# Optimization experiments

Measured on AMD Instinct MI355X. Metric: run time of the kernel, lower is better.

The kernel has to match this reference:

```python
import jax, jax.numpy as jnp
import numpy as np
import math

OUT_H, OUT_W = 608 // 4, 1088 // 4   # 152, 272
HW = OUT_H * OUT_W                   # 41344
MAX_OBJS = 256
N_ANN = 64
NID = 537
EMB_DIM = 256
EMB_SCALE = math.sqrt(2.0) * math.log(NID - 1.0)
B = 8


def gaussian_radius(height, width, min_overlap=0.7):
    # standard CenterNet radius; height/width are jnp.ceil'd box sizes
    b1 = height + width
    c1 = width * height * (1.0 - min_overlap) / (1.0 + min_overlap)
    r1 = (b1 + jnp.sqrt(jnp.maximum(b1 * b1 - 4.0 * c1, 0.0))) / 2.0
    b2 = 2.0 * (height + width)
    c2 = (1.0 - min_overlap) * width * height
    r2 = (b2 + jnp.sqrt(jnp.maximum(b2 * b2 - 16.0 * c2, 0.0))) / 2.0
    b3 = -2.0 * min_overlap * (height + width)
    c3 = (min_overlap - 1.0) * width * height
    r3 = (b3 + jnp.sqrt(jnp.maximum(b3 * b3 - 16.0 * min_overlap * c3, 0.0))) / 2.0
    return jnp.minimum(jnp.minimum(r1, r2), r3)


def build_targets(ann1, ann2):
    # ann cols: [cx, cy, w, h, cls, pid, vis, extra]; boxes normalized to [0,1]
    cx_raw = ann1[:, 0] * OUT_W
    cy_raw = ann1[:, 1] * OUT_H
    w = ann1[:, 2] * OUT_W
    h = ann1[:, 3] * OUT_H
    # amodal box from UNclipped center (torch deepcopies before clipping)
    x1 = cx_raw - 0.5 * w; y1 = cy_raw - 0.5 * h
    x2 = x1 + w;           y2 = y1 + h
    cx = jnp.clip(cx_raw, 0.0, OUT_W - 1.0)
    cy = jnp.clip(cy_raw, 0.0, OUT_H - 1.0)
    ctx = cx.astype(jnp.int32)
    cty = cy.astype(jnp.int32)
    radius = jnp.maximum(jnp.floor(gaussian_radius(jnp.ceil(h), jnp.ceil(w))), 0.0)

    # batched gaussian splat, max-reduced over objects (draw_umich_gaussian)
    sigma = (2.0 * radius + 1.0) / 6.0
    dx = jnp.arange(OUT_W, dtype=jnp.float32)[None, :] - ctx[:, None].astype(jnp.float32)  # [N,W]
    dy = jnp.arange(OUT_H, dtype=jnp.float32)[None, :] - cty[:, None].astype(jnp.float32)  # [N,H]
    g = jnp.exp(-(dy[:, :, None] ** 2 + dx[:, None, :] ** 2) / (2.0 * sigma[:, None, None] ** 2))  # [N,H,W]
    win = (jnp.abs(dy)[:, :, None] <= radius[:, None, None]) & (jnp.abs(dx)[:, None, :] <= radius[:, None, None])
    hm = jnp.max(jnp.where(win, g, 0.0), axis=0)  # [H,W]

    # first match of each object's pid in the next frame (torch breaks at first hit)
    pid1 = ann1[:, 5]
    match = pid1[:, None] == ann2[None, :, 5]
    has = match.any(axis=1)
    t1 = ann2[jnp.argmax(match, axis=1)]
    cx2 = t1[:, 0] * OUT_W; cy2 = t1[:, 1] * OUT_H
    w2 = t1[:, 2] * OUT_W;  h2 = t1[:, 3] * OUT_H
    x1t = cx2 - 0.5 * w2; y1t = cy2 - 0.5 * h2
    x2t = x1t + w2;       y2t = y1t + h2

    valid = has & (h > 0) & (w > 0) & (h2 > 0) & (w2 > 0)
    vm = valid.astype(jnp.float32)
    cxf = ctx.astype(jnp.float32); cyf = cty.astype(jnp.float32)
    wh = jnp.stack([cxf - x1, x2 - cxf, cyf - y1, y2 - cyf,
                    cxf - x1t, x2t - cxf, cyf - y1t, y2t - cyf], axis=-1) * vm[:, None]
    ind = jnp.where(valid, cty * OUT_W + ctx, 0)
    v = ann1[:, 6] * vm
    ids = jnp.where(valid, pid1.astype(jnp.int32), 0)

    pad = MAX_OBJS - N_ANN
    return (hm,
            jnp.pad(ind, (0, pad)),
            jnp.pad(vm, (0, pad)),
            jnp.pad(wh, ((0, pad), (0, 0))),
            jnp.pad(v, (0, pad)),
            jnp.pad(ids, (0, pad)))


def focal_loss(pred, gt):
    # CenterNet focal loss; pred already sigmoid+clamped
    pos = (gt == 1.0).astype(pred.dtype)
    pos_loss = (jnp.log(pred) * (1.0 - pred) ** 2 * pos).sum()
    neg_loss = (jnp.log(1.0 - pred) * pred ** 2 * (1.0 - gt) ** 4 * (1.0 - pos)).sum()
    num_pos = pos.sum()
    return jnp.where(num_pos > 0, -(pos_loss + neg_loss) / jnp.maximum(num_pos, 1.0), -neg_loss)


def reg_loss(feat, mask, ind, target):
    # feat [C,HW]; gather per-object channels, masked smooth-L1 sum / num_valid
    pred = feat[:, ind].T                       # [max_objs, C]
    m = mask[:, None]
    d = jnp.abs(pred * m - target * m)
    sl1 = jnp.where(d < 1.0, 0.5 * d * d, d - 0.5)
    return sl1.sum() / (mask.sum() + 1e-4)


def id_loss(identi, ind, mask, v, ids, W_id, b_id):
    feat = identi[:, ind].T                     # [max_objs, 256]
    feat = EMB_SCALE * feat / jnp.maximum(jnp.linalg.norm(feat, axis=-1, keepdims=True), 1e-12)
    logits = feat @ W_id.T + b_id               # [max_objs, 537]
    logp = jax.nn.log_softmax(logits, axis=-1)
    nll = -v * jnp.take_along_axis(logp, ids[:, None], axis=1)[:, 0]
    return (nll * mask).sum() / jnp.maximum(mask.sum(), 1.0)


def reference(classifications, regressions, viss, identis, annotations1, annotations2, W_id, b_id, s_det, s_id):
    cls = jnp.clip(jax.nn.sigmoid(classifications), 1e-4, 1.0 - 1e-4)   # [B,1,HW]
    vis = jnp.clip(jax.nn.sigmoid(viss), 1e-4, 1.0 - 1e-4)              # [B,1,HW]
    hm, ind, mask, wh, v, ids = jax.vmap(build_targets)(annotations1, annotations2)
    cls_l = jax.vmap(lambda p, g: focal_loss(p.reshape(OUT_H, OUT_W), g))(cls, hm)
    reg_l = jax.vmap(reg_loss)(regressions, mask, ind, wh)
    vis_l = jax.vmap(lambda f, m, i, t: reg_loss(f, m, i, t[:, None]))(vis, mask, ind, v)
    id_l = jax.vmap(lambda f, i, m, vv, ii: id_loss(f, i, m, vv, ii, W_id, b_id))(identis, ind, mask, v, ids)
    return (cls_l.mean(keepdims=True), reg_l.mean(keepdims=True), vis_l.mean(keepdims=True),
            id_l.mean(keepdims=True), s_det, s_id)


def setup_inputs() -> dict:
    key = jax.random.key(0)
    ks = jax.random.split(key, 8)
    classifications = jax.random.normal(ks[0], (B, 1, HW), dtype=jnp.float32)
    regressions = jax.random.normal(ks[1], (B, 8, HW), dtype=jnp.float32)
    viss = jax.random.normal(ks[2], (B, 1, HW), dtype=jnp.float32)
    identis = jax.random.normal(ks[3], (B, EMB_DIM, HW), dtype=jnp.float32)

    def make_frame_pair(k):
        k1, k2, k3, k4, k5, k6, k7 = jax.random.split(k, 7)
        cx = jax.random.uniform(k1, (N_ANN,), minval=0.05, maxval=0.95)
        cy = jax.random.uniform(k2, (N_ANN,), minval=0.05, maxval=0.95)
        w = jax.random.uniform(k3, (N_ANN,), minval=0.02, maxval=0.25)
        h = jax.random.uniform(k4, (N_ANN,), minval=0.05, maxval=0.4)
        pid = jax.random.permutation(k5, NID)[:N_ANN].astype(jnp.float32)  # unique track ids
        vis = jax.random.uniform(k6, (N_ANN,))
        extra = jax.random.uniform(k7, (N_ANN,))
        cls = jnp.zeros((N_ANN,), dtype=jnp.float32)
        a1 = jnp.stack([cx, cy, w, h, cls, pid, vis, extra], axis=-1)
        kp, kj = jax.random.split(jax.random.fold_in(k, 99))
        a2 = a1[jax.random.permutation(kp, N_ANN)]
        a2 = a2.at[:, 0:2].add(0.01 * jax.random.normal(kj, (N_ANN, 2)))
        a2 = a2.at[:, 0:2].set(jnp.clip(a2[:, 0:2], 0.05, 0.95))
        return a1, a2

    pairs = [make_frame_pair(jax.random.fold_in(ks[4], b)) for b in range(B)]
    annotations1 = jnp.stack([p[0] for p in pairs])
    annotations2 = jnp.stack([p[1] for p in pairs])
    W_id = 0.02 * jax.random.normal(ks[5], (NID, EMB_DIM), dtype=jnp.float32)
    b_id = jnp.zeros((NID,), dtype=jnp.float32)
    s_det = jnp.array([-1.85], dtype=jnp.float32)
    s_id = jnp.array([-1.05], dtype=jnp.float32)
    return {"classifications": classifications, "regressions": regressions, "viss": viss,
            "identis": identis, "annotations1": annotations1, "annotations2": annotations2,
            "W_id": W_id, "b_id": b_id, "s_det": s_det, "s_id": s_id}
```

## Files before the change

kernel.cpp:

```cpp
#include <hip/hip_runtime.h>
#include <math.h>

#define OUT_H 152
#define OUT_W 272
#define HW 41344
#define NOBJ 64
#define NB 8
#define NID 537
#define EMB 256

#define NFBLK 162
#define NFOCAL (NFBLK * NB)
#define NIDBLK (NB * NOBJ)

#define OF_FP    0
#define OF_IDNLL (NFOCAL * 3)
#define OF_REGP  (OF_IDNLL + 512)
#define OF_VISP  (OF_REGP + 512)
#define OF_VMV   (OF_VISP + 512)

__device__ inline float waveRedSum(float v) {
  for (int off = 32; off; off >>= 1) v += __shfl_down(v, off, 64);
  return v;
}
__device__ inline float waveRedMax(float v) {
  for (int off = 32; off; off >>= 1) v = fmaxf(v, __shfl_down(v, off, 64));
  return v;
}

struct PrepOut {
  float cxf, cyf, radius, inv2s2, vm, v;
  float wh[8];
  int ind, id;
};

__device__ __forceinline__ PrepOut prep_obj(const float* __restrict__ ann1,
                                            const float* __restrict__ ann2,
                                            int b, int i) {
  const float* a1 = ann1 + (b * NOBJ + i) * 8;
  const float* A2 = ann2 + b * NOBJ * 8;

  float cx_raw = a1[0] * (float)OUT_W;
  float cy_raw = a1[1] * (float)OUT_H;
  float w = a1[2] * (float)OUT_W;
  float h = a1[3] * (float)OUT_H;
  float x1 = cx_raw - 0.5f * w, y1 = cy_raw - 0.5f * h;
  float x2 = x1 + w, y2 = y1 + h;
  float cx = fminf(fmaxf(cx_raw, 0.f), (float)(OUT_W - 1));
  float cy = fminf(fmaxf(cy_raw, 0.f), (float)(OUT_H - 1));
  int ctx = (int)cx, cty = (int)cy;

  float hc = ceilf(h), wc = ceilf(w);
  float b1 = hc + wc;
  float c1 = wc * hc * 0.3f / 1.7f;
  float r1 = (b1 + sqrtf(fmaxf(b1 * b1 - 4.f * c1, 0.f))) * 0.5f;
  float b2 = 2.f * (hc + wc);
  float c2 = 0.3f * wc * hc;
  float r2 = (b2 + sqrtf(fmaxf(b2 * b2 - 16.f * c2, 0.f))) * 0.5f;
  float b3 = -1.4f * (hc + wc);
  float c3 = -0.3f * wc * hc;
  float r3 = (b3 + sqrtf(fmaxf(b3 * b3 - 11.2f * c3, 0.f))) * 0.5f;
  float radius = fmaxf(floorf(fminf(fminf(r1, r2), r3)), 0.f);
  float sigma = (2.f * radius + 1.f) / 6.f;

  PrepOut P;
  P.cxf = (float)ctx;
  P.cyf = (float)cty;
  P.radius = radius;
  P.inv2s2 = 1.f / (2.f * sigma * sigma);

  float pid = a1[5];
  int jm = -1;
  for (int j = 0; j < NOBJ; ++j) {
    if (A2[j * 8 + 5] == pid) { jm = j; break; }
  }
  bool has = (jm >= 0);
  const float* t1 = A2 + (has ? jm : 0) * 8;
  float cx2 = t1[0] * (float)OUT_W, cy2 = t1[1] * (float)OUT_H;
  float w2 = t1[2] * (float)OUT_W, h2 = t1[3] * (float)OUT_H;
  float x1t = cx2 - 0.5f * w2, y1t = cy2 - 0.5f * h2;
  float x2t = x1t + w2, y2t = y1t + h2;

  bool valid = has && (h > 0.f) && (w > 0.f) && (h2 > 0.f) && (w2 > 0.f);
  float vm = valid ? 1.f : 0.f;
  P.vm = vm;
  P.v = a1[6] * vm;
  P.wh[0] = (P.cxf - x1) * vm;  P.wh[1] = (x2 - P.cxf) * vm;
  P.wh[2] = (P.cyf - y1) * vm;  P.wh[3] = (y2 - P.cyf) * vm;
  P.wh[4] = (P.cxf - x1t) * vm; P.wh[5] = (x2t - P.cxf) * vm;
  P.wh[6] = (P.cyf - y1t) * vm; P.wh[7] = (y2t - P.cyf) * vm;
  P.ind = valid ? (cty * OUT_W + ctx) : 0;
  P.id = valid ? (int)pid : 0;
  return P;
}

__global__ void __launch_bounds__(256)
main_kernel(const float* __restrict__ cls,
            const float* __restrict__ reg,
            const float* __restrict__ viss,
            const float* __restrict__ identis,
            const float* __restrict__ W_id,
            const float* __restrict__ b_id,
            const float* __restrict__ ann1,
            const float* __restrict__ ann2,
            float* __restrict__ F) {
  if (blockIdx.x < NFOCAL) {
    int blk = blockIdx.x;
    int b = blk / NFBLK;
    int bx = blk - b * NFBLK;
    int p = bx * 256 + threadIdx.x;

    __shared__ float s_ctx[64], s_cty[64], s_rad[64], s_inv[64];
    if (threadIdx.x < 64) {
      PrepOut P = prep_obj(ann1, ann2, b, threadIdx.x);
      s_ctx[threadIdx.x] = P.cxf;
      s_cty[threadIdx.x] = P.cyf;
      s_rad[threadIdx.x] = P.radius;
      s_inv[threadIdx.x] = P.inv2s2;
    }
    __syncthreads();

    float pos_l = 0.f, neg_l = 0.f, npos = 0.f;
    if (p < HW) {
      float xf = (float)(p % OUT_W);
      float yf = (float)(p / OUT_W);
      float gt = 0.f;
      #pragma unroll 8
      for (int o = 0; o < 64; ++o) {
        float dy = yf - s_cty[o];
        float dx = xf - s_ctx[o];
        float r = s_rad[o];
        if (fabsf(dy) <= r && fabsf(dx) <= r) {
          gt = fmaxf(gt, expf(-(dy * dy + dx * dx) * s_inv[o]));
        }
      }
      float x = cls[b * HW + p];
      float pr = 1.f / (1.f + expf(-x));
      pr = fminf(fmaxf(pr, 1e-4f), 0.9999f);
      if (gt == 1.f) {
        float om = 1.f - pr;
        pos_l = logf(pr) * om * om;
        npos = 1.f;
      } else {
        float omg = 1.f - gt;
        float w4 = omg * omg;
        w4 *= w4;
        neg_l = logf(1.f - pr) * pr * pr * w4;
      }
    }

    __shared__ float red[3][4];
    int wid = threadIdx.x >> 6, lane = threadIdx.x & 63;
    float a = waveRedSum(pos_l);
    float c = waveRedSum(neg_l);
    float n = waveRedSum(npos);
    if (lane == 0) { red[0][wid] = a; red[1][wid] = c; red[2][wid] = n; }
    __syncthreads();
    if (threadIdx.x == 0) {
      float pa = 0.f, pc = 0.f, pn = 0.f;
      for (int k = 0; k < 4; ++k) { pa += red[0][k]; pc += red[1][k]; pn += red[2][k]; }
      F[OF_FP + blk * 3 + 0] = pa;
      F[OF_FP + blk * 3 + 1] = pc;
      F[OF_FP + blk * 3 + 2] = pn;
    }
  } else {
    int o = blockIdx.x - NFOCAL;
    int b = o >> 6, i = o & 63;
    int t = threadIdx.x;
    int wid = t >> 6, lane = t & 63;
    PrepOut P = prep_obj(ann1, ann2, b, i);

    if (wid == 0) {
      float rv = 0.f, vv = 0.f;
      if (lane < 8) {
        float pred = reg[(b * 8 + lane) * HW + P.ind];
        float d = fabsf(pred * P.vm - P.wh[lane]);
        rv = (d < 1.f) ? 0.5f * d * d : d - 0.5f;
      } else if (lane == 8) {
        float s = 1.f / (1.f + expf(-viss[b * HW + P.ind]));
        s = fminf(fmaxf(s, 1e-4f), 0.9999f);
        float d = fabsf(s * P.vm - P.v);
        vv = (d < 1.f) ? 0.5f * d * d : d - 0.5f;
      }
      rv = waveRedSum(rv);
      vv = waveRedSum(vv);
      if (lane == 0) {
        F[OF_REGP + o] = rv;
        F[OF_VISP + o] = vv;
        F[OF_VMV + o]  = P.vm;
      }
    }

    if (P.vm == 0.f) {
      if (t == 0) F[OF_IDNLL + o] = 0.f;
      return;
    }

    __shared__ float shf[EMB];
    __shared__ float slog[544];
    __shared__ float red4[4];

    float f = identis[(size_t)b * EMB * HW + (size_t)t * HW + P.ind];
    float n2 = waveRedSum(f * f);
    if (lane == 0) red4[wid] = n2;
    __syncthreads();
    float norm2 = red4[0] + red4[1] + red4[2] + red4[3];
    const float EMB_SCALE = 1.41421356237309515f * logf(536.0f);
    float scale = EMB_SCALE / fmaxf(sqrtf(norm2), 1e-12f);
    shf[t] = f * scale;
    __syncthreads();

    float4 s4 = *(const float4*)&shf[lane * 4];
    for (int r0 = wid * 4; r0 < NID; r0 += 16) {
      float acc[4];
      #pragma unroll
      for (int rr = 0; rr < 4; ++rr) {
        int r = r0 + rr;
        float ax = 0.f;
        if (r < NID) {
          const float4 wv = *(const float4*)&W_id[(size_t)r * EMB + lane * 4];
          ax = wv.x * s4.x + wv.y * s4.y + wv.z * s4.z + wv.w * s4.w;
        }
        acc[rr] = ax;
      }
      #pragma unroll
      for (int rr = 0; rr < 4; ++rr)
        for (int off = 32; off; off >>= 1)
          acc[rr] += __shfl_down(acc[rr], off, 64);
      if (lane == 0) {
        #pragma unroll
        for (int rr = 0; rr < 4; ++rr) {
          int r = r0 + rr;
          if (r < NID) slog[r] = acc[rr] + b_id[r];
        }
      }
    }
    __syncthreads();

    float mx = -1e30f;
    for (int c = t; c < NID; c += 256) mx = fmaxf(mx, slog[c]);
    mx = waveRedMax(mx);
    __syncthreads();
    if (lane == 0) red4[wid] = mx;
    __syncthreads();
    mx = fmaxf(fmaxf(red4[0], red4[1]), fmaxf(red4[2], red4[3]));

    float se = 0.f;
    for (int c = t; c < NID; c += 256) se += expf(slog[c] - mx);
    se = waveRedSum(se);
    __syncthreads();
    if (lane == 0) red4[wid] = se;
    __syncthreads();

    if (t == 0) {
      float sesum = red4[0] + red4[1] + red4[2] + red4[3];
      float lse = mx + logf(sesum);
      F[OF_IDNLL + o] = -P.v * (slog[P.id] - lse);
    }
  }
}

__global__ void __launch_bounds__(512)
final_kernel(const float* __restrict__ F,
             const float* __restrict__ s_det,
             const float* __restrict__ s_id,
             float* __restrict__ out) {
  int t = threadIdx.x;
  int b = t >> 6;
  int lane = t & 63;

  float pa = 0.f, pc = 0.f, pn = 0.f;
  for (int e = lane; e < NFBLK; e += 64) {
    const float* fp = F + OF_FP + (b * NFBLK + e) * 3;
    pa += fp[0]; pc += fp[1]; pn += fp[2];
  }
  pa = waveRedSum(pa);
  pc = waveRedSum(pc);
  pn = waveRedSum(pn);

  float rsum = waveRedSum(F[OF_REGP + b * 64 + lane]);
  float vsum = waveRedSum(F[OF_VISP + b * 64 + lane]);
  float msum = waveRedSum(F[OF_VMV  + b * 64 + lane]);
  float idv  = waveRedSum(F[OF_IDNLL + b * 64 + lane]);

  __shared__ float L[8][4];
  if (lane == 0) {
    L[b][0] = (pn > 0.f) ? (-(pa + pc) / fmaxf(pn, 1.f)) : (-pc);
    L[b][1] = rsum / (msum + 0.0001f);
    L[b][2] = vsum / (msum + 0.0001f);
    L[b][3] = idv / fmaxf(msum, 1.f);
  }
  __syncthreads();
  if (t == 0) {
    float cl = 0.f, rl = 0.f, vl = 0.f, il = 0.f;
    for (int k = 0; k < 8; ++k) {
      cl += L[k][0]; rl += L[k][1]; vl += L[k][2]; il += L[k][3];
    }
    out[0] = cl / 8.f;
    out[1] = rl / 8.f;
    out[2] = vl / 8.f;
    out[3] = il / 8.f;
    out[4] = s_det[0];
    out[5] = s_id[0];
  }
}

extern "C" void kernel_launch(void* const* d_in, const int* in_sizes, int n_in,
                              void* d_out, int out_size, void* d_ws, size_t ws_size,
                              hipStream_t stream) {
  const float* cls     = (const float*)d_in[0];
  const float* reg     = (const float*)d_in[1];
  const float* viss    = (const float*)d_in[2];
  const float* identis = (const float*)d_in[3];
  const float* ann1    = (const float*)d_in[4];
  const float* ann2    = (const float*)d_in[5];
  const float* W_id    = (const float*)d_in[6];
  const float* b_id    = (const float*)d_in[7];
  const float* s_det   = (const float*)d_in[8];
  const float* s_id    = (const float*)d_in[9];
  float* F = (float*)d_ws;

  main_kernel<<<NFOCAL + NIDBLK, 256, 0, stream>>>(cls, reg, viss, identis,
                                                   W_id, b_id, ann1, ann2, F);
  final_kernel<<<1, 512, 0, stream>>>(F, s_det, s_id, (float*)d_out);
}
```

Baseline: 69.48 us.

## Fuse final reduction into main kernel via last-block atomic counter

Removes the separate final_kernel launch: each block increments a global counter after its work, and the last block to finish performs the cross-batch reduction and writes the outputs. ID blocks are moved to the front of the grid so the longer embedding/GEMV work starts first. The ID GEMV loop is restructured so 16 lanes cover each row with four float4 loads, leaving four rows per wave per iteration and a shorter xor-shuffle reduction. A hipMemsetAsync is added to reset the counter each call, which itself adds a small stream operation.

Result: slower. 81.44 us (+17.2%).

```diff
diff --git a/kernel.cpp b/kernel.cpp
--- a/kernel.cpp
+++ b/kernel.cpp
@@ -9,12 +9,13 @@
 #define NID 537
 #define EMB 256
 
+#define NIDBLK 512
 #define NFBLK 162
 #define NFOCAL (NFBLK * NB)
-#define NIDBLK (NB * NOBJ)
-
-#define OF_FP    0
-#define OF_IDNLL (NFOCAL * 3)
+#define NBLOCKS (NIDBLK + NFOCAL)
+
+#define OF_FP    16
+#define OF_IDNLL (OF_FP + NFOCAL * 3)
 #define OF_REGP  (OF_IDNLL + 512)
 #define OF_VISP  (OF_REGP + 512)
 #define OF_VMV   (OF_VISP + 512)
@@ -103,20 +104,118 @@
             const float* __restrict__ b_id,
             const float* __restrict__ ann1,
             const float* __restrict__ ann2,
-            float* __restrict__ F) {
-  if (blockIdx.x < NFOCAL) {
-    int blk = blockIdx.x;
+            const float* __restrict__ s_det,
+            const float* __restrict__ s_id,
+            float* __restrict__ F,
+            float* __restrict__ out) {
+  int t = threadIdx.x;
+  int wid = t >> 6, lane = t & 63;
+
+  if (blockIdx.x < NIDBLK) {
+    int o = blockIdx.x;
+    int b = o >> 6, i = o & 63;
+    PrepOut P = prep_obj(ann1, ann2, b, i);
+
+    if (wid == 0) {
+      float rv = 0.f, vv = 0.f;
+      if (lane < 8) {
+        float pred = reg[(b * 8 + lane) * HW + P.ind];
+        float d = fabsf(pred * P.vm - P.wh[lane]);
+        rv = (d < 1.f) ? 0.5f * d * d : d - 0.5f;
+      } else if (lane == 8) {
+        float s = 1.f / (1.f + expf(-viss[b * HW + P.ind]));
+        s = fminf(fmaxf(s, 1e-4f), 0.9999f);
+        float d = fabsf(s * P.vm - P.v);
+        vv = (d < 1.f) ? 0.5f * d * d : d - 0.5f;
+      }
+      rv = waveRedSum(rv);
+      vv = waveRedSum(vv);
+      if (lane == 0) {
+        F[OF_REGP + o] = rv;
+        F[OF_VISP + o] = vv;
+        F[OF_VMV + o]  = P.vm;
+      }
+    }
+
+    if (P.vm == 0.f) {
+      if (t == 0) F[OF_IDNLL + o] = 0.f;
+    } else {
+      __shared__ float shf[EMB];
+      __shared__ float slog[544];
+      __shared__ float red4[4];
+
+      float f = identis[(size_t)b * EMB * HW + (size_t)t * HW + P.ind];
+      float n2 = waveRedSum(f * f);
+      if (lane == 0) red4[wid] = n2;
+      __syncthreads();
+      float norm2 = red4[0] + red4[1] + red4[2] + red4[3];
+      const float EMB_SCALE = 1.41421356237309515f * logf(536.0f);
+      float scale = EMB_SCALE / fmaxf(sqrtf(norm2), 1e-12f);
+      shf[t] = f * scale;
+      __syncthreads();
+
+      int g = lane >> 4, j = lane & 15;
+      float4 e0 = *(const float4*)&shf[j * 4];
+      float4 e1 = *(const float4*)&shf[j * 4 + 64];
+      float4 e2 = *(const float4*)&shf[j * 4 + 128];
+      float4 e3 = *(const float4*)&shf[j * 4 + 192];
+      for (int it = 0; it < 34; ++it) {
+        int r = wid * 4 + it * 16 + g;
+        bool ok = (r < NID);
+        float acc = 0.f;
+        if (ok) {
+          const float* wr = W_id + (size_t)r * EMB + j * 4;
+          float4 w0 = *(const float4*)(wr);
+          float4 w1 = *(const float4*)(wr + 64);
+          float4 w2 = *(const float4*)(wr + 128);
+          float4 w3 = *(const float4*)(wr + 192);
+          acc = w0.x * e0.x + w0.y * e0.y + w0.z * e0.z + w0.w * e0.w
+              + w1.x * e1.x + w1.y * e1.y + w1.z * e1.z + w1.w * e1.w
+              + w2.x * e2.x + w2.y * e2.y + w2.z * e2.z + w2.w * e2.w
+              + w3.x * e3.x + w3.y * e3.y + w3.z * e3.z + w3.w * e3.w;
+        }
+        acc += __shfl_xor(acc, 8, 64);
+        acc += __shfl_xor(acc, 4, 64);
+        acc += __shfl_xor(acc, 2, 64);
+        acc += __shfl_xor(acc, 1, 64);
+        if (ok && j == 0) slog[r] = acc + b_id[r];
+      }
+      __syncthreads();
+
+      float mx = -1e30f;
+      for (int c = t; c < NID; c += 256) mx = fmaxf(mx, slog[c]);
+      mx = waveRedMax(mx);
+      __syncthreads();
+      if (lane == 0) red4[wid] = mx;
+      __syncthreads();
+      mx = fmaxf(fmaxf(red4[0], red4[1]), fmaxf(red4[2], red4[3]));
+
+      float se = 0.f;
+      for (int c = t; c < NID; c += 256) se += expf(slog[c] - mx);
+      se = waveRedSum(se);
+      __syncthreads();
+      if (lane == 0) red4[wid] = se;
+      __syncthreads();
+
+      if (t == 0) {
+        float sesum = red4[0] + red4[1] + red4[2] + red4[3];
+        float lse = mx + logf(sesum);
+        F[OF_IDNLL + o] = -P.v * (slog[P.id] - lse);
+      }
+    }
+  } else {
+    int blk = blockIdx.x - NIDBLK;
     int b = blk / NFBLK;
     int bx = blk - b * NFBLK;
-    int p = bx * 256 + threadIdx.x;
+    int p = bx * 256 + t;
 
     __shared__ float s_ctx[64], s_cty[64], s_rad[64], s_inv[64];
-    if (threadIdx.x < 64) {
-      PrepOut P = prep_obj(ann1, ann2, b, threadIdx.x);
-      s_ctx[threadIdx.x] = P.cxf;
-      s_cty[threadIdx.x] = P.cyf;
-      s_rad[threadIdx.x] = P.radius;
-      s_inv[threadIdx.x] = P.inv2s2;
+    if (t < 64) {
+      PrepOut P = prep_obj(ann1, ann2, b, t);
+      s_ctx[t] = P.cxf;
+      s_cty[t] = P.cyf;
+      s_rad[t] = P.radius;
+      s_inv[t] = P.inv2s2;
     }
     __syncthreads();
 
@@ -150,158 +249,64 @@
     }
 
     __shared__ float red[3][4];
-    int wid = threadIdx.x >> 6, lane = threadIdx.x & 63;
     float a = waveRedSum(pos_l);
     float c = waveRedSum(neg_l);
     float n = waveRedSum(npos);
     if (lane == 0) { red[0][wid] = a; red[1][wid] = c; red[2][wid] = n; }
     __syncthreads();
-    if (threadIdx.x == 0) {
+    if (t == 0) {
       float pa = 0.f, pc = 0.f, pn = 0.f;
       for (int k = 0; k < 4; ++k) { pa += red[0][k]; pc += red[1][k]; pn += red[2][k]; }
       F[OF_FP + blk * 3 + 0] = pa;
       F[OF_FP + blk * 3 + 1] = pc;
       F[OF_FP + blk * 3 + 2] = pn;
     }
-  } else {
-    int o = blockIdx.x - NFOCAL;
-    int b = o >> 6, i = o & 63;
-    int t = threadIdx.x;
-    int wid = t >> 6, lane = t & 63;
-    PrepOut P = prep_obj(ann1, ann2, b, i);
-
-    if (wid == 0) {
-      float rv = 0.f, vv = 0.f;
-      if (lane < 8) {
-        float pred = reg[(b * 8 + lane) * HW + P.ind];
-        float d = fabsf(pred * P.vm - P.wh[lane]);
-        rv = (d < 1.f) ? 0.5f * d * d : d - 0.5f;
-      } else if (lane == 8) {
-        float s = 1.f / (1.f + expf(-viss[b * HW + P.ind]));
-        s = fminf(fmaxf(s, 1e-4f), 0.9999f);
-        float d = fabsf(s * P.vm - P.v);
-        vv = (d < 1.f) ? 0.5f * d * d : d - 0.5f;
-      }
-      rv = waveRedSum(rv);
-      vv = waveRedSum(vv);
-      if (lane == 0) {
-        F[OF_REGP + o] = rv;
-        F[OF_VISP + o] = vv;
-        F[OF_VMV + o]  = P.vm;
-      }
-    }
-
-    if (P.vm == 0.f) {
-      if (t == 0) F[OF_IDNLL + o] = 0.f;
-      return;
-    }
-
-    __shared__ float shf[EMB];
-    __shared__ float slog[544];
-    __shared__ float red4[4];
-
-    float f = identis[(size_t)b * EMB * HW + (size_t)t * HW + P.ind];
-    float n2 = waveRedSum(f * f);
-    if (lane == 0) red4[wid] = n2;
-    __syncthreads();
-    float norm2 = red4[0] + red4[1] + red4[2] + red4[3];
-    const float EMB_SCALE = 1.41421356237309515f * logf(536.0f);
-    float scale = EMB_SCALE / fmaxf(sqrtf(norm2), 1e-12f);
-    shf[t] = f * scale;
-    __syncthreads();
-
-    float4 s4 = *(const float4*)&shf[lane * 4];
-    for (int r0 = wid * 4; r0 < NID; r0 += 16) {
-      float acc[4];
-      #pragma unroll
-      for (int rr = 0; rr < 4; ++rr) {
-        int r = r0 + rr;
-        float ax = 0.f;
-        if (r < NID) {
-          const float4 wv = *(const float4*)&W_id[(size_t)r * EMB + lane * 4];
-          ax = wv.x * s4.x + wv.y * s4.y + wv.z * s4.z + wv.w * s4.w;
-        }
-        acc[rr] = ax;
-      }
-      #pragma unroll
-      for (int rr = 0; rr < 4; ++rr)
-        for (int off = 32; off; off >>= 1)
-          acc[rr] += __shfl_down(acc[rr], off, 64);
-      if (lane == 0) {
-        #pragma unroll
-        for (int rr = 0; rr < 4; ++rr) {
-          int r = r0 + rr;
-          if (r < NID) slog[r] = acc[rr] + b_id[r];
-        }
-      }
-    }
-    __syncthreads();
-
-    float mx = -1e30f;
-    for (int c = t; c < NID; c += 256) mx = fmaxf(mx, slog[c]);
-    mx = waveRedMax(mx);
-    __syncthreads();
-    if (lane == 0) red4[wid] = mx;
-    __syncthreads();
-    mx = fmaxf(fmaxf(red4[0], red4[1]), fmaxf(red4[2], red4[3]));
-
-    float se = 0.f;
-    for (int c = t; c < NID; c += 256) se += expf(slog[c] - mx);
-    se = waveRedSum(se);
-    __syncthreads();
-    if (lane == 0) red4[wid] = se;
-    __syncthreads();
-
-    if (t == 0) {
-      float sesum = red4[0] + red4[1] + red4[2] + red4[3];
-      float lse = mx + logf(sesum);
-      F[OF_IDNLL + o] = -P.v * (slog[P.id] - lse);
-    }
   }
-}
-
-__global__ void __launch_bounds__(512)
-final_kernel(const float* __restrict__ F,
-             const float* __restrict__ s_det,
-             const float* __restrict__ s_id,
-             float* __restrict__ out) {
-  int t = threadIdx.x;
-  int b = t >> 6;
-  int lane = t & 63;
-
-  float pa = 0.f, pc = 0.f, pn = 0.f;
-  for (int e = lane; e < NFBLK; e += 64) {
-    const float* fp = F + OF_FP + (b * NFBLK + e) * 3;
-    pa += fp[0]; pc += fp[1]; pn += fp[2];
-  }
-  pa = waveRedSum(pa);
-  pc = waveRedSum(pc);
-  pn = waveRedSum(pn);
-
-  float rsum = waveRedSum(F[OF_REGP + b * 64 + lane]);
-  float vsum = waveRedSum(F[OF_VISP + b * 64 + lane]);
-  float msum = waveRedSum(F[OF_VMV  + b * 64 + lane]);
-  float idv  = waveRedSum(F[OF_IDNLL + b * 64 + lane]);
-
-  __shared__ float L[8][4];
-  if (lane == 0) {
-    L[b][0] = (pn > 0.f) ? (-(pa + pc) / fmaxf(pn, 1.f)) : (-pc);
-    L[b][1] = rsum / (msum + 0.0001f);
-    L[b][2] = vsum / (msum + 0.0001f);
-    L[b][3] = idv / fmaxf(msum, 1.f);
+
+  __syncthreads();
+  __shared__ unsigned s_old;
+  if (t == 0) {
+    __threadfence();
+    s_old = atomicAdd((unsigned*)F, 1u);
   }
   __syncthreads();
-  if (t == 0) {
-    float cl = 0.f, rl = 0.f, vl = 0.f, il = 0.f;
-    for (int k = 0; k < 8; ++k) {
-      cl += L[k][0]; rl += L[k][1]; vl += L[k][2]; il += L[k][3];
-    }
-    out[0] = cl / 8.f;
-    out[1] = rl / 8.f;
-    out[2] = vl / 8.f;
-    out[3] = il / 8.f;
-    out[4] = s_det[0];
-    out[5] = s_id[0];
+  if (s_old == NBLOCKS - 1) {
+    __threadfence();
+    __shared__ float L[8][4];
+    for (int half = 0; half < 2; ++half) {
+      int b = wid * 2 + half;
+      float pa = 0.f, pc = 0.f, pn = 0.f;
+      for (int e = lane; e < NFBLK; e += 64) {
+        const float* fp = F + OF_FP + (b * NFBLK + e) * 3;
+        pa += fp[0]; pc += fp[1]; pn += fp[2];
+      }
+      pa = waveRedSum(pa);
+      pc = waveRedSum(pc);
+      pn = waveRedSum(pn);
+      float rs = waveRedSum(F[OF_REGP + b * 64 + lane]);
+      float vs = waveRedSum(F[OF_VISP + b * 64 + lane]);
+      float ms = waveRedSum(F[OF_VMV  + b * 64 + lane]);
+      float iv = waveRedSum(F[OF_IDNLL + b * 64 + lane]);
+      if (lane == 0) {
+        L[b][0] = (pn > 0.f) ? (-(pa + pc) / fmaxf(pn, 1.f)) : (-pc);
+        L[b][1] = rs / (ms + 0.0001f);
+        L[b][2] = vs / (ms + 0.0001f);
+        L[b][3] = iv / fmaxf(ms, 1.f);
+      }
+    }
+    __syncthreads();
+    if (t == 0) {
+      float cl = 0.f, rl = 0.f, vl = 0.f, il = 0.f;
+      for (int k = 0; k < 8; ++k) {
+        cl += L[k][0]; rl += L[k][1]; vl += L[k][2]; il += L[k][3];
+      }
+      out[0] = cl / 8.f;
+      out[1] = rl / 8.f;
+      out[2] = vl / 8.f;
+      out[3] = il / 8.f;
+      out[4] = s_det[0];
+      out[5] = s_id[0];
+    }
   }
 }
 
@@ -320,7 +325,8 @@
   const float* s_id    = (const float*)d_in[9];
   float* F = (float*)d_ws;
 
-  main_kernel<<<NFOCAL + NIDBLK, 256, 0, stream>>>(cls, reg, viss, identis,
-                                                   W_id, b_id, ann1, ann2, F);
-  final_kernel<<<1, 512, 0, stream>>>(F, s_det, s_id, (float*)d_out);
-}
+  hipMemsetAsync(d_ws, 0, 4, stream);
+  main_kernel<<<NBLOCKS, 256, 0, stream>>>(cls, reg, viss, identis,
+                                           W_id, b_id, ann1, ann2,
+                                           s_det, s_id, F, (float*)d_out);
+}
```
